# Kernel tuning notes

Hardware: AMD Instinct MI355X
Metric: run time of the kernel (lower is better)

## Reference

```python
import jax, jax.numpy as jnp
import numpy as np


def _sq_dist(q, k):
    # pairwise squared L2 distance: [B,H,L,D] x [B,H,M,D] -> [B,H,L,M]
    q2 = jnp.sum(q * q, axis=-1)[..., :, None]
    k2 = jnp.sum(k * k, axis=-1)[..., None, :]
    qk = jnp.einsum('bhld,bhmd->bhlm', q, k)
    return q2 + k2 - 2.0 * qk


def setup_inputs() -> dict:
    key = jax.random.key(0)
    k1, k2, k3 = jax.random.split(key, 3)
    B, H, L, D = 2, 8, 2048, 64
    query = jax.random.normal(k1, (B, H, L, D), dtype=jnp.float32)
    key_t = jax.random.normal(k2, (B, H, L, D), dtype=jnp.float32)
    mask = jnp.ones((B, L), dtype=jnp.float32)
    # mu param: normal(0, 0.5) * [0,1][:,None,None] -> first component zeroed
    mu = (jax.random.normal(k3, (2, H, D), dtype=jnp.float32) * 0.5
          * jnp.array([0.0, 1.0], dtype=jnp.float32)[:, None, None])
    pi = jnp.array([0.5, 0.5], dtype=jnp.float32)
    return {'query': query, 'key': key_t, 'mask': mask, 'mu': mu, 'pi': pi}


def reference(query, key, mask, mu, pi):
    D = query.shape[-1]
    var = D ** 0.5  # self.var = head_dim ** 0.5
    neg = 1e6 * (1.0 - mask[:, None, None, :])  # [B,1,1,L]
    pic = jnp.clip(pi, 0.0, 1.0)
    qk1 = (-0.5 / var) * _sq_dist(query, key - mu[0][None, :, None, :]) - neg
    qk2 = (-0.5 / var) * _sq_dist(query, key - mu[1][None, :, None, :]) - neg
    attn = jnp.exp(qk1) * pic[0] + jnp.exp(qk2) * pic[1]
    return attn / jnp.sum(attn, axis=-1, keepdims=True)
```

## Files before the change

### kernel.cpp

```cpp
#include <hip/hip_runtime.h>
#include <math.h>

#define B_ 2
#define H_ 8
#define L_ 2048
#define D_ 64
#define BM 64
#define BN 128
#define NJ (L_ / BN)
#define NT 512
#define L2E 1.4426950408889634f

typedef __attribute__((ext_vector_type(8))) short short8;
typedef __attribute__((ext_vector_type(4))) float f4;

typedef __attribute__((address_space(3))) void lds_void_t;
typedef const __attribute__((address_space(1))) void gbl_void_t;
#define GLL16(gp, lp) __builtin_amdgcn_global_load_lds( \
    (gbl_void_t*)(gp), (lds_void_t*)(lp), 16, 0, 0)

#define MFMA16(a, b, c) __builtin_amdgcn_mfma_f32_16x16x32_bf16(a, b, c, 0, 0, 0)

struct LdsT {
  short8 kth[BN * 8];
  short8 ktl[BN * 8];
  float2 cka[L_];
  float  muv[2][D_];
  float  er0[BM], er1[BM];
  float  red[4][BM];
};

__device__ inline void split8(const float4& a0, const float4& a1,
                              short8& hi, short8& lo) {
  float xs[8] = {a0.x, a0.y, a0.z, a0.w, a1.x, a1.y, a1.z, a1.w};
#pragma unroll
  for (int e = 0; e < 8; ++e) {
    unsigned u  = __float_as_uint(xs[e]);
    unsigned hb = (u + 0x8000u) & 0xFFFF0000u;
    float    r  = xs[e] - __uint_as_float(hb);
    unsigned lb = (__float_as_uint(r) + 0x8000u) >> 16;
    hi[e] = (short)(hb >> 16);
    lo[e] = (short)lb;
  }
}

__global__ __launch_bounds__(256) void prep_kernel(
    const float* __restrict__ k, const float* __restrict__ mask,
    const float* __restrict__ mu, float2* __restrict__ ck,
    short8* __restrict__ wh, short8* __restrict__ wl)
{
  int bh = blockIdx.x >> 3;
  int c  = (blockIdx.x & 7) * 256 + threadIdx.x;
  int b  = bh >> 3, h = bh & 7;
  const float s = -0.0625f;
  const float* kp  = k  + ((size_t)bh * L_ + c) * D_;
  const float* mu0 = mu + (size_t)h * D_;
  const float* mu1 = mu + (size_t)(H_ * D_) + (size_t)h * D_;
  float x[D_];
#pragma unroll
  for (int d = 0; d < D_; d += 4)
    *reinterpret_cast<float4*>(&x[d]) = *reinterpret_cast<const float4*>(kp + d);
  float s0 = 0.f, s1 = 0.f;
#pragma unroll
  for (int d = 0; d < D_; ++d) {
    float a = x[d] - mu0[d]; s0 += a * a;
    float bb = x[d] - mu1[d]; s1 += bb * bb;
  }
  float neg = 1.0e6f * (1.0f - mask[(size_t)b * L_ + c]);
  ck[(size_t)bh * L_ + c] = make_float2(exp2f((s * s0 - neg) * L2E),
                                        exp2f((s * s1 - neg) * L2E));
#pragma unroll
  for (int gp = 0; gp < 8; ++gp) {
    int g = gp ^ (c & 7);
    short8 hi, lo;
    split8(*reinterpret_cast<const float4*>(&x[8 * g]),
           *reinterpret_cast<const float4*>(&x[8 * g + 4]), hi, lo);
    size_t idx = ((size_t)bh * L_ + c) * 8 + gp;
    wh[idx] = hi;
    wl[idx] = lo;
  }
}

template <bool USE_WS>
__global__ __launch_bounds__(NT, 2) void mg_kernel(
    const float* __restrict__ q, const float* __restrict__ kk,
    const float* __restrict__ mask, const float* __restrict__ mu,
    const float* __restrict__ pi, const float2* __restrict__ ckw,
    const short8* __restrict__ wh, const short8* __restrict__ wl,
    float* __restrict__ out)
{
  extern __shared__ __align__(16) char smem_raw[];
  LdsT& S = *reinterpret_cast<LdsT*>(smem_raw);
  const int t = threadIdx.x;
  int bid = blockIdx.x;
  int vwg = (bid & 7) * 64 + (bid >> 3);
  int bh  = vwg >> 5;
  int rb  = vwg & 31;
  int b = bh >> 3, h = bh & 7;
  int row0 = rb * BM;

  const int w  = t >> 6;
  const int ln = t & 63;
  const int ci = ln & 15;
  const int kg = ln >> 4;
  const int x7 = ci & 7;
  const int wc = w & 3;
  const int wr = (w >> 2) * 32;

  const float s   = -0.0625f;
  const float DDC = 0.125f * L2E;

  const float*  maskb = mask + (size_t)b * L_;
  const float2* ckb   = ckw + (size_t)bh * L_;
  const float4* kb4   = (const float4*)(kk + (size_t)bh * L_ * D_);
  const short8* whb   = wh + (size_t)bh * (L_ * 8);
  const short8* wlb   = wl + (size_t)bh * (L_ * 8);

  if (t < 2 * D_)
    S.muv[t >> 6][t & 63] =
        mu[(size_t)(t >> 6) * (H_ * D_) + (size_t)h * D_ + (t & 63)];

  if (USE_WS) {
#pragma unroll
    for (int i = 0; i < 4; ++i) {
      int u = t + NT * i;
      S.cka[u] = ckb[u];
    }
  }

  short8 ah[2][2], al[2][2];
#pragma unroll
  for (int rk = 0; rk < 2; ++rk) {
    const float* qrow = q + ((size_t)bh * L_ + row0 + wr + rk * 16 + ci) * D_;
#pragma unroll
    for (int h2 = 0; h2 < 2; ++h2) {
      float4 a0 = *reinterpret_cast<const float4*>(qrow + 32 * h2 + kg * 8);
      float4 a1 = *reinterpret_cast<const float4*>(qrow + 32 * h2 + kg * 8 + 4);
      split8(a0, a1, ah[rk][h2], al[rk][h2]);
    }
  }
  __syncthreads();

  if (t < BM) {
    float pi0 = fminf(fmaxf(pi[0], 0.f), 1.f);
    float pi1 = fminf(fmaxf(pi[1], 0.f), 1.f);
    const float* qr = q + ((size_t)bh * L_ + row0 + t) * D_;
    float a0 = 0.f, a1 = 0.f, a2 = 0.f;
#pragma unroll
    for (int dq = 0; dq < 16; ++dq) {
      float4 qv = *reinterpret_cast<const float4*>(qr + 4 * dq);
      a0 += qv.x * qv.x + qv.y * qv.y + qv.z * qv.z + qv.w * qv.w;
      a1 += qv.x * S.muv[0][4*dq] + qv.y * S.muv[0][4*dq+1] +
            qv.z * S.muv[0][4*dq+2] + qv.w * S.muv[0][4*dq+3];
      a2 += qv.x * S.muv[1][4*dq] + qv.y * S.muv[1][4*dq+1] +
            qv.z * S.muv[1][4*dq+2] + qv.w * S.muv[1][4*dq+3];
    }
    S.er0[t] = pi0 * exp2f((s * a0 + 2.f * s * a1) * L2E);
    S.er1[t] = pi1 * exp2f((s * a0 + 2.f * s * a2) * L2E);
  }
  __syncthreads();

  float e0r[2][4], e1r[2][4];
#pragma unroll
  for (int rk = 0; rk < 2; ++rk)
#pragma unroll
    for (int reg = 0; reg < 4; ++reg) {
      e0r[rk][reg] = S.er0[wr + rk * 16 + kg * 4 + reg];
      e1r[rk][reg] = S.er1[wr + rk * 16 + kg * 4 + reg];
    }

  auto STAGE = [&](int j) {
    if (USE_WS) {
#pragma unroll
      for (int i = 0; i < 2; ++i)
        GLL16(whb + (size_t)j * (BN * 8) + t + NT * i, &S.kth[t + NT * i]);
#pragma unroll
      for (int i = 0; i < 2; ++i)
        GLL16(wlb + (size_t)j * (BN * 8) + t + NT * i, &S.ktl[t + NT * i]);
    } else {
#pragma unroll
      for (int i = 0; i < 2; ++i) {
        int u = t + NT * i;
        int col = u >> 3, gp = u & 7, g = gp ^ (col & 7);
        float4 x0 = kb4[(size_t)(j * BN + col) * 16 + 2 * g];
        float4 x1 = kb4[(size_t)(j * BN + col) * 16 + 2 * g + 1];
        short8 hi, lo;
        split8(x0, x1, hi, lo);
        S.kth[u] = hi;
        S.ktl[u] = lo;
      }
      if (t < BN) {
        const float* kc = kk + ((size_t)bh * L_ + j * BN + t) * D_;
        float s0 = 0.f, s1 = 0.f;
#pragma unroll
        for (int dq = 0; dq < 16; ++dq) {
          float4 kv = *reinterpret_cast<const float4*>(kc + 4 * dq);
          float a;
          a = kv.x - S.muv[0][4*dq];   s0 += a * a;
          a = kv.y - S.muv[0][4*dq+1]; s0 += a * a;
          a = kv.z - S.muv[0][4*dq+2]; s0 += a * a;
          a = kv.w - S.muv[0][4*dq+3]; s0 += a * a;
          a = kv.x - S.muv[1][4*dq];   s1 += a * a;
          a = kv.y - S.muv[1][4*dq+1]; s1 += a * a;
          a = kv.z - S.muv[1][4*dq+2]; s1 += a * a;
          a = kv.w - S.muv[1][4*dq+3]; s1 += a * a;
        }
        float neg = 1.0e6f * (1.0f - maskb[j * BN + t]);
        S.cka[j * BN + t] = make_float2(exp2f((s * s0 - neg) * L2E),
                                        exp2f((s * s1 - neg) * L2E));
      }
    }
  };

  float rsum[2][4] = {{0.f, 0.f, 0.f, 0.f}, {0.f, 0.f, 0.f, 0.f}};
#pragma unroll 1
  for (int j = 0; j < NJ; ++j) {
    __syncthreads();
    STAGE(j);
    __syncthreads();
    float2 ec[2];
#pragma unroll
    for (int n = 0; n < 2; ++n)
      ec[n] = S.cka[j * BN + wc * 32 + 16 * n + ci];
#pragma unroll
    for (int n = 0; n < 2; ++n) {
      int base = (wc * 32 + n * 16 + ci) * 8;
      short8 b0h = S.kth[base + (kg ^ x7)];
      short8 b1h = S.kth[base + ((4 + kg) ^ x7)];
      short8 b0l = S.ktl[base + (kg ^ x7)];
      short8 b1l = S.ktl[base + ((4 + kg) ^ x7)];
#pragma unroll
      for (int rk = 0; rk < 2; ++rk) {
        f4 acc = {0.f, 0.f, 0.f, 0.f};
        acc = MFMA16(ah[rk][0], b0h, acc);
        acc = MFMA16(ah[rk][1], b1h, acc);
        acc = MFMA16(ah[rk][0], b0l, acc);
        acc = MFMA16(ah[rk][1], b1l, acc);
        acc = MFMA16(al[rk][0], b0h, acc);
        acc = MFMA16(al[rk][1], b1h, acc);
#pragma unroll
        for (int reg = 0; reg < 4; ++reg) {
          float g2 = __builtin_amdgcn_exp2f(DDC * acc[reg]);
          float m  = fmaf(e0r[rk][reg], ec[n].x, e1r[rk][reg] * ec[n].y);
          rsum[rk][reg] = fmaf(g2, m, rsum[rk][reg]);
        }
      }
    }
  }

#pragma unroll
  for (int rk = 0; rk < 2; ++rk)
#pragma unroll
    for (int reg = 0; reg < 4; ++reg) {
      float v = rsum[rk][reg];
      v += __shfl_xor(v, 1, 64);
      v += __shfl_xor(v, 2, 64);
      v += __shfl_xor(v, 4, 64);
      v += __shfl_xor(v, 8, 64);
      if (ci == 0) S.red[wc][wr + rk * 16 + kg * 4 + reg] = v;
    }
  __syncthreads();
#pragma unroll
  for (int rk = 0; rk < 2; ++rk)
#pragma unroll
    for (int reg = 0; reg < 4; ++reg) {
      int r = wr + rk * 16 + kg * 4 + reg;
      float inv = 1.0f / (S.red[0][r] + S.red[1][r] + S.red[2][r] + S.red[3][r]);
      e0r[rk][reg] *= inv;
      e1r[rk][reg] *= inv;
    }

  float* ob = out + ((size_t)bh * L_ + row0 + wr + kg * 4) * L_ + wc * 32 + ci;
#pragma unroll 1
  for (int jj = 0; jj < NJ; ++jj) {
    const int j = NJ - 1 - jj;
    if (jj != 0) {
      __syncthreads();
      STAGE(j);
      __syncthreads();
    }
    float2 ec[2];
#pragma unroll
    for (int n = 0; n < 2; ++n)
      ec[n] = S.cka[j * BN + wc * 32 + 16 * n + ci];
#pragma unroll
    for (int n = 0; n < 2; ++n) {
      int base = (wc * 32 + n * 16 + ci) * 8;
      short8 b0h = S.kth[base + (kg ^ x7)];
      short8 b1h = S.kth[base + ((4 + kg) ^ x7)];
      short8 b0l = S.ktl[base + (kg ^ x7)];
      short8 b1l = S.ktl[base + ((4 + kg) ^ x7)];
#pragma unroll
      for (int rk = 0; rk < 2; ++rk) {
        f4 acc = {0.f, 0.f, 0.f, 0.f};
        acc = MFMA16(ah[rk][0], b0h, acc);
        acc = MFMA16(ah[rk][1], b1h, acc);
        acc = MFMA16(ah[rk][0], b0l, acc);
        acc = MFMA16(ah[rk][1], b1l, acc);
        acc = MFMA16(al[rk][0], b0h, acc);
        acc = MFMA16(al[rk][1], b1h, acc);
#pragma unroll
        for (int reg = 0; reg < 4; ++reg) {
          float g2 = __builtin_amdgcn_exp2f(DDC * acc[reg]);
          float m  = fmaf(e0r[rk][reg], ec[n].x, e1r[rk][reg] * ec[n].y);
          float p  = g2 * m;
          __builtin_nontemporal_store(
              p, ob + (size_t)(rk * 16 + reg) * L_ + (j * BN + n * 16));
        }
      }
    }
  }
}

extern "C" void kernel_launch(void* const* d_in, const int* in_sizes, int n_in,
                              void* d_out, int out_size, void* d_ws, size_t ws_size,
                              hipStream_t stream) {
  const float* q    = (const float*)d_in[0];
  const float* k    = (const float*)d_in[1];
  const float* mask = (const float*)d_in[2];
  const float* mu   = (const float*)d_in[3];
  const float* pi   = (const float*)d_in[4];
  float* out = (float*)d_out;

  const size_t smem     = sizeof(LdsT);
  const size_t ck_bytes = (size_t)B_ * H_ * L_ * sizeof(float2);
  const size_t wp_bytes = (size_t)B_ * H_ * L_ * D_ * sizeof(short);
  const bool use_ws = (ws_size >= ck_bytes + 2 * wp_bytes) && (d_ws != nullptr);

  if (use_ws) {
    float2* ck = (float2*)d_ws;
    short8* wh = (short8*)((char*)d_ws + ck_bytes);
    short8* wl = (short8*)((char*)d_ws + ck_bytes + wp_bytes);
    (void)hipFuncSetAttribute(reinterpret_cast<const void*>(&mg_kernel<true>),
                              hipFuncAttributeMaxDynamicSharedMemorySize, (int)smem);
    prep_kernel<<<dim3(B_ * H_ * 8), dim3(256), 0, stream>>>(k, mask, mu, ck, wh, wl);
    mg_kernel<true><<<dim3(B_ * H_ * (L_ / BM)), dim3(NT), smem, stream>>>(
        q, k, mask, mu, pi, ck, wh, wl, out);
  } else {
    (void)hipFuncSetAttribute(reinterpret_cast<const void*>(&mg_kernel<false>),
                              hipFuncAttributeMaxDynamicSharedMemorySize, (int)smem);
    mg_kernel<false><<<dim3(B_ * H_ * (L_ / BM)), dim3(NT), smem, stream>>>(
        q, k, mask, mu, pi, nullptr, nullptr, nullptr, out);
  }
}
```

Before: 121.6 us.

## Replace split-bf16 three-pass MFMA with single fp16 MFMA and halve row tile

```diff
diff --git a/kernel.cpp b/kernel.cpp
--- a/kernel.cpp
+++ b/kernel.cpp
@@ -5,13 +5,13 @@
 #define H_ 8
 #define L_ 2048
 #define D_ 64
-#define BM 64
+#define BM 32
 #define BN 128
 #define NJ (L_ / BN)
 #define NT 512
 #define L2E 1.4426950408889634f
 
-typedef __attribute__((ext_vector_type(8))) short short8;
+typedef _Float16 half8 __attribute__((ext_vector_type(8)));
 typedef __attribute__((ext_vector_type(4))) float f4;
 
 typedef __attribute__((address_space(3))) void lds_void_t;
@@ -19,35 +19,29 @@
 #define GLL16(gp, lp) __builtin_amdgcn_global_load_lds( \
     (gbl_void_t*)(gp), (lds_void_t*)(lp), 16, 0, 0)
 
-#define MFMA16(a, b, c) __builtin_amdgcn_mfma_f32_16x16x32_bf16(a, b, c, 0, 0, 0)
+#define MFMA16F(a, b, c) __builtin_amdgcn_mfma_f32_16x16x32_f16(a, b, c, 0, 0, 0)
 
 struct LdsT {
-  short8 kth[BN * 8];
-  short8 ktl[BN * 8];
+  half8  kth[BN * 8];
   float2 cka[L_];
   float  muv[2][D_];
   float  er0[BM], er1[BM];
   float  red[4][BM];
 };
 
-__device__ inline void split8(const float4& a0, const float4& a1,
-                              short8& hi, short8& lo) {
-  float xs[8] = {a0.x, a0.y, a0.z, a0.w, a1.x, a1.y, a1.z, a1.w};
-#pragma unroll
-  for (int e = 0; e < 8; ++e) {
-    unsigned u  = __float_as_uint(xs[e]);
-    unsigned hb = (u + 0x8000u) & 0xFFFF0000u;
-    float    r  = xs[e] - __uint_as_float(hb);
-    unsigned lb = (__float_as_uint(r) + 0x8000u) >> 16;
-    hi[e] = (short)(hb >> 16);
-    lo[e] = (short)lb;
-  }
+__device__ inline half8 cvt8(const float4& a0, const float4& a1) {
+  half8 r;
+  r[0] = (_Float16)a0.x; r[1] = (_Float16)a0.y;
+  r[2] = (_Float16)a0.z; r[3] = (_Float16)a0.w;
+  r[4] = (_Float16)a1.x; r[5] = (_Float16)a1.y;
+  r[6] = (_Float16)a1.z; r[7] = (_Float16)a1.w;
+  return r;
 }
 
 __global__ __launch_bounds__(256) void prep_kernel(
     const float* __restrict__ k, const float* __restrict__ mask,
     const float* __restrict__ mu, float2* __restrict__ ck,
-    short8* __restrict__ wh, short8* __restrict__ wl)
+    half8* __restrict__ wh)
 {
   int bh = blockIdx.x >> 3;
   int c  = (blockIdx.x & 7) * 256 + threadIdx.x;
@@ -72,30 +66,26 @@
 #pragma unroll
   for (int gp = 0; gp < 8; ++gp) {
     int g = gp ^ (c & 7);
-    short8 hi, lo;
-    split8(*reinterpret_cast<const float4*>(&x[8 * g]),
-           *reinterpret_cast<const float4*>(&x[8 * g + 4]), hi, lo);
-    size_t idx = ((size_t)bh * L_ + c) * 8 + gp;
-    wh[idx] = hi;
-    wl[idx] = lo;
+    wh[((size_t)bh * L_ + c) * 8 + gp] =
+        cvt8(*reinterpret_cast<const float4*>(&x[8 * g]),
+             *reinterpret_cast<const float4*>(&x[8 * g + 4]));
   }
 }
 
 template <bool USE_WS>
-__global__ __launch_bounds__(NT, 2) void mg_kernel(
+__global__ __launch_bounds__(NT, 8) void mg_kernel(
     const float* __restrict__ q, const float* __restrict__ kk,
     const float* __restrict__ mask, const float* __restrict__ mu,
     const float* __restrict__ pi, const float2* __restrict__ ckw,
-    const short8* __restrict__ wh, const short8* __restrict__ wl,
-    float* __restrict__ out)
+    const half8* __restrict__ wh, float* __restrict__ out)
 {
   extern __shared__ __align__(16) char smem_raw[];
   LdsT& S = *reinterpret_cast<LdsT*>(smem_raw);
   const int t = threadIdx.x;
   int bid = blockIdx.x;
-  int vwg = (bid & 7) * 64 + (bid >> 3);
-  int bh  = vwg >> 5;
-  int rb  = vwg & 31;
+  int vwg = (bid & 7) * 128 + (bid >> 3);
+  int bh  = vwg >> 6;
+  int rb  = vwg & 63;
   int b = bh >> 3, h = bh & 7;
   int row0 = rb * BM;
 
@@ -105,7 +95,7 @@
   const int kg = ln >> 4;
   const int x7 = ci & 7;
   const int wc = w & 3;
-  const int wr = (w >> 2) * 32;
+  const int wr = (w >> 2) * 16;
 
   const float s   = -0.0625f;
   const float DDC = 0.125f * L2E;
@@ -113,8 +103,7 @@
   const float*  maskb = mask + (size_t)b * L_;
   const float2* ckb   = ckw + (size_t)bh * L_;
   const float4* kb4   = (const float4*)(kk + (size_t)bh * L_ * D_);
-  const short8* whb   = wh + (size_t)bh * (L_ * 8);
-  const short8* wlb   = wl + (size_t)bh * (L_ * 8);
+  const half8*  whb   = wh + (size_t)bh * (L_ * 8);
 
   if (t < 2 * D_)
     S.muv[t >> 6][t & 63] =
@@ -128,15 +117,14 @@
     }
   }
 
-  short8 ah[2][2], al[2][2];
-#pragma unroll
-  for (int rk = 0; rk < 2; ++rk) {
-    const float* qrow = q + ((size_t)bh * L_ + row0 + wr + rk * 16 + ci) * D_;
+  half8 ah[2];
+  {
+    const float* qrow = q + ((size_t)bh * L_ + row0 + wr + ci) * D_;
 #pragma unroll
     for (int h2 = 0; h2 < 2; ++h2) {
       float4 a0 = *reinterpret_cast<const float4*>(qrow + 32 * h2 + kg * 8);
       float4 a1 = *reinterpret_cast<const float4*>(qrow + 32 * h2 + kg * 8 + 4);
-      split8(a0, a1, ah[rk][h2], al[rk][h2]);
+      ah[h2] = cvt8(a0, a1);
     }
   }
   __syncthreads();
@@ -160,23 +148,18 @@
   }
   __syncthreads();
 
-  float e0r[2][4], e1r[2][4];
-#pragma unroll
-  for (int rk = 0; rk < 2; ++rk)
-#pragma unroll
-    for (int reg = 0; reg < 4; ++reg) {
-      e0r[rk][reg] = S.er0[wr + rk * 16 + kg * 4 + reg];
-      e1r[rk][reg] = S.er1[wr + rk * 16 + kg * 4 + reg];
-    }
+  float e0r[4], e1r[4];
+#pragma unroll
+  for (int reg = 0; reg < 4; ++reg) {
+    e0r[reg] = S.er0[wr + kg * 4 + reg];
+    e1r[reg] = S.er1[wr + kg * 4 + reg];
+  }
 
   auto STAGE = [&](int j) {
     if (USE_WS) {
 #pragma unroll
       for (int i = 0; i < 2; ++i)
         GLL16(whb + (size_t)j * (BN * 8) + t + NT * i, &S.kth[t + NT * i]);
-#pragma unroll
-      for (int i = 0; i < 2; ++i)
-        GLL16(wlb + (size_t)j * (BN * 8) + t + NT * i, &S.ktl[t + NT * i]);
     } else {
 #pragma unroll
       for (int i = 0; i < 2; ++i) {
@@ -184,10 +167,7 @@
         int col = u >> 3, gp = u & 7, g = gp ^ (col & 7);
         float4 x0 = kb4[(size_t)(j * BN + col) * 16 + 2 * g];
         float4 x1 = kb4[(size_t)(j * BN + col) * 16 + 2 * g + 1];
-        short8 hi, lo;
-        split8(x0, x1, hi, lo);
-        S.kth[u] = hi;
-        S.ktl[u] = lo;
+        S.kth[u] = cvt8(x0, x1);
       }
       if (t < BN) {
         const float* kc = kk + ((size_t)bh * L_ + j * BN + t) * D_;
@@ -212,7 +192,7 @@
     }
   };
 
-  float rsum[2][4] = {{0.f, 0.f, 0.f, 0.f}, {0.f, 0.f, 0.f, 0.f}};
+  float rsum[4] = {0.f, 0.f, 0.f, 0.f};
 #pragma unroll 1
   for (int j = 0; j < NJ; ++j) {
     __syncthreads();
@@ -225,50 +205,37 @@
 #pragma unroll
     for (int n = 0; n < 2; ++n) {
       int base = (wc * 32 + n * 16 + ci) * 8;
-      short8 b0h = S.kth[base + (kg ^ x7)];
-      short8 b1h = S.kth[base + ((4 + kg) ^ x7)];
-      short8 b0l = S.ktl[base + (kg ^ x7)];
-      short8 b1l = S.ktl[base + ((4 + kg) ^ x7)];
-#pragma unroll
-      for (int rk = 0; rk < 2; ++rk) {
-        f4 acc = {0.f, 0.f, 0.f, 0.f};
-        acc = MFMA16(ah[rk][0], b0h, acc);
-        acc = MFMA16(ah[rk][1], b1h, acc);
-        acc = MFMA16(ah[rk][0], b0l, acc);
-        acc = MFMA16(ah[rk][1], b1l, acc);
-        acc = MFMA16(al[rk][0], b0h, acc);
-        acc = MFMA16(al[rk][1], b1h, acc);
-#pragma unroll
-        for (int reg = 0; reg < 4; ++reg) {
-          float g2 = __builtin_amdgcn_exp2f(DDC * acc[reg]);
-          float m  = fmaf(e0r[rk][reg], ec[n].x, e1r[rk][reg] * ec[n].y);
-          rsum[rk][reg] = fmaf(g2, m, rsum[rk][reg]);
-        }
+      half8 b0 = S.kth[base + (kg ^ x7)];
+      half8 b1 = S.kth[base + ((4 + kg) ^ x7)];
+      f4 acc = {0.f, 0.f, 0.f, 0.f};
+      acc = MFMA16F(ah[0], b0, acc);
+      acc = MFMA16F(ah[1], b1, acc);
+#pragma unroll
+      for (int reg = 0; reg < 4; ++reg) {
+        float g2 = __builtin_amdgcn_exp2f(DDC * acc[reg]);
+        float m  = fmaf(e0r[reg], ec[n].x, e1r[reg] * ec[n].y);
+        rsum[reg] = fmaf(g2, m, rsum[reg]);
       }
     }
   }
 
 #pragma unroll
-  for (int rk = 0; rk < 2; ++rk)
-#pragma unroll
-    for (int reg = 0; reg < 4; ++reg) {
-      float v = rsum[rk][reg];
-      v += __shfl_xor(v, 1, 64);
-      v += __shfl_xor(v, 2, 64);
-      v += __shfl_xor(v, 4, 64);
-      v += __shfl_xor(v, 8, 64);
-      if (ci == 0) S.red[wc][wr + rk * 16 + kg * 4 + reg] = v;
-    }
+  for (int reg = 0; reg < 4; ++reg) {
+    float v = rsum[reg];
+    v += __shfl_xor(v, 1, 64);
+    v += __shfl_xor(v, 2, 64);
+    v += __shfl_xor(v, 4, 64);
+    v += __shfl_xor(v, 8, 64);
+    if (ci == 0) S.red[wc][wr + kg * 4 + reg] = v;
+  }
   __syncthreads();
 #pragma unroll
-  for (int rk = 0; rk < 2; ++rk)
-#pragma unroll
-    for (int reg = 0; reg < 4; ++reg) {
-      int r = wr + rk * 16 + kg * 4 + reg;
-      float inv = 1.0f / (S.red[0][r] + S.red[1][r] + S.red[2][r] + S.red[3][r]);
-      e0r[rk][reg] *= inv;
-      e1r[rk][reg] *= inv;
-    }
+  for (int reg = 0; reg < 4; ++reg) {
+    int r = wr + kg * 4 + reg;
+    float inv = 1.0f / (S.red[0][r] + S.red[1][r] + S.red[2][r] + S.red[3][r]);
+    e0r[reg] *= inv;
+    e1r[reg] *= inv;
+  }
 
   float* ob = out + ((size_t)bh * L_ + row0 + wr + kg * 4) * L_ + wc * 32 + ci;
 #pragma unroll 1
@@ -286,27 +253,18 @@
 #pragma unroll
     for (int n = 0; n < 2; ++n) {
       int base = (wc * 32 + n * 16 + ci) * 8;
-      short8 b0h = S.kth[base + (kg ^ x7)];
-      short8 b1h = S.kth[base + ((4 + kg) ^ x7)];
-      short8 b0l = S.ktl[base + (kg ^ x7)];
-      short8 b1l = S.ktl[base + ((4 + kg) ^ x7)];
-#pragma unroll
-      for (int rk = 0; rk < 2; ++rk) {
-        f4 acc = {0.f, 0.f, 0.f, 0.f};
-        acc = MFMA16(ah[rk][0], b0h, acc);
-        acc = MFMA16(ah[rk][1], b1h, acc);
-        acc = MFMA16(ah[rk][0], b0l, acc);
-        acc = MFMA16(ah[rk][1], b1l, acc);
-        acc = MFMA16(al[rk][0], b0h, acc);
-        acc = MFMA16(al[rk][1], b1h, acc);
-#pragma unroll
-        for (int reg = 0; reg < 4; ++reg) {
-          float g2 = __builtin_amdgcn_exp2f(DDC * acc[reg]);
-          float m  = fmaf(e0r[rk][reg], ec[n].x, e1r[rk][reg] * ec[n].y);
-          float p  = g2 * m;
-          __builtin_nontemporal_store(
-              p, ob + (size_t)(rk * 16 + reg) * L_ + (j * BN + n * 16));
-        }
+      half8 b0 = S.kth[base + (kg ^ x7)];
+      half8 b1 = S.kth[base + ((4 + kg) ^ x7)];
+      f4 acc = {0.f, 0.f, 0.f, 0.f};
+      acc = MFMA16F(ah[0], b0, acc);
+      acc = MFMA16F(ah[1], b1, acc);
+#pragma unroll
+      for (int reg = 0; reg < 4; ++reg) {
+        float g2 = __builtin_amdgcn_exp2f(DDC * acc[reg]);
+        float m  = fmaf(e0r[reg], ec[n].x, e1r[reg] * ec[n].y);
+        float p  = g2 * m;
+        __builtin_nontemporal_store(
+            p, ob + (size_t)reg * L_ + (j * BN + n * 16));
       }
     }
   }
@@ -325,21 +283,20 @@
   const size_t smem     = sizeof(LdsT);
   const size_t ck_bytes = (size_t)B_ * H_ * L_ * sizeof(float2);
   const size_t wp_bytes = (size_t)B_ * H_ * L_ * D_ * sizeof(short);
-  const bool use_ws = (ws_size >= ck_bytes + 2 * wp_bytes) && (d_ws != nullptr);
+  const bool use_ws = (ws_size >= ck_bytes + wp_bytes) && (d_ws != nullptr);
 
   if (use_ws) {
     float2* ck = (float2*)d_ws;
-    short8* wh = (short8*)((char*)d_ws + ck_bytes);
-    short8* wl = (short8*)((char*)d_ws + ck_bytes + wp_bytes);
+    half8*  wh = (half8*)((char*)d_ws + ck_bytes);
     (void)hipFuncSetAttribute(reinterpret_cast<const void*>(&mg_kernel<true>),
                               hipFuncAttributeMaxDynamicSharedMemorySize, (int)smem);
-    prep_kernel<<<dim3(B_ * H_ * 8), dim3(256), 0, stream>>>(k, mask, mu, ck, wh, wl);
+    prep_kernel<<<dim3(B_ * H_ * 8), dim3(256), 0, stream>>>(k, mask, mu, ck, wh);
     mg_kernel<true><<<dim3(B_ * H_ * (L_ / BM)), dim3(NT), smem, stream>>>(
-        q, k, mask, mu, pi, ck, wh, wl, out);
+        q, k, mask, mu, pi, ck, wh, out);
   } else {
     (void)hipFuncSetAttribute(reinterpret_cast<const void*>(&mg_kernel<false>),
                               hipFuncAttributeMaxDynamicSharedMemorySize, (int)smem);
     mg_kernel<false><<<dim3(B_ * H_ * (L_ / BM)), dim3(NT), smem, stream>>>(
-        q, k, mask, mu, pi, nullptr, nullptr, nullptr, out);
+        q, k, mask, mu, pi, nullptr, nullptr, out);
   }
 }
```

Result: faster. 114.0 us (-6.3%).
